# Kernel tuning notes

Hardware: AMD Instinct MI355X
Metric: run time of the kernel (lower is better)

## Reference

```python
import math
import jax, jax.numpy as jnp
import numpy as np

B, D, E, R, TOP_K = 16384, 2048, 64, 128, 2
TAU = 1.0
CAP_FACTOR = 1.25
TOP_C = min(E, max(4, 2 * TOP_K))  # GatingNetwork default top_c


def setup_inputs() -> dict:
    key = jax.random.key(0)
    ks = jax.random.split(key, 7)
    x = jax.random.normal(ks[0], (B, D), dtype=jnp.float32)
    # shared_encoder: nn.Linear(d, d) -> weight [out, in], bias [out]
    We = jax.random.normal(ks[1], (D, D), dtype=jnp.float32) / np.sqrt(D)
    be = jnp.zeros((D,), dtype=jnp.float32)
    # gating: nn.Linear(d, E, bias=False) -> weight [E, d]
    Wg = jax.random.normal(ks[2], (E, D), dtype=jnp.float32) / np.sqrt(D)
    # LowRankExpert per expert: U [r, d], V [d, r], gamma scalar (init 1.0)
    U = jax.random.normal(ks[3], (E, R, D), dtype=jnp.float32) / np.sqrt(D)
    V = jax.random.normal(ks[4], (E, D, R), dtype=jnp.float32) / np.sqrt(R)
    gamma = jnp.ones((E,), dtype=jnp.float32)
    return {"x": x, "We": We, "be": be, "Wg": Wg, "U": U, "V": V, "gamma": gamma}


def reference(x, We, be, Wg, U, V, gamma):
    # shared encoder
    enc = x @ We.T + be  # [B, D]

    # ---- gating: top-C candidates then top-K routing ----
    logits = (enc @ Wg.T) / TAU  # [B, E]
    topc_vals, topc_idx = jax.lax.top_k(logits, TOP_C)          # [B, C]
    topk_vals, pos_in_c = jax.lax.top_k(topc_vals, TOP_K)       # [B, K]
    topk_idx = jnp.take_along_axis(topc_idx, pos_in_c, axis=1)  # [B, K]
    # masked stable softmax over the K selected logits (with 1e-12 eps as in source)
    m = jnp.max(topk_vals, axis=-1, keepdims=True)
    ex = jnp.exp(topk_vals - m)
    w = ex / (jnp.sum(ex, axis=-1, keepdims=True) + 1e-12)      # [B, K]

    # ---- flatten assignments ----
    N = B * TOP_K
    tok = jnp.repeat(jnp.arange(B), TOP_K)   # [N]
    eid = topk_idx.reshape(-1)               # [N]
    wf = w.reshape(-1)                       # [N]
    wmask = wf > 1e-12

    # ---- capacity-based dispatch (sort/group equivalent, fixed shapes) ----
    cap = int(math.ceil(CAP_FACTOR * N / E))  # expert capacity
    onehot = ((eid[:, None] == jnp.arange(E)[None, :]) & wmask[:, None]).astype(jnp.int32)  # [N, E]
    pos = jnp.cumsum(onehot, axis=0) - onehot                      # position within expert
    pos_of = jnp.take_along_axis(pos, eid[:, None], axis=1)[:, 0]  # [N]
    valid = wmask & (pos_of < cap)
    slot = jnp.where(valid, pos_of, cap)  # overflow -> dummy slot (never occurs at this cap)

    # gather tokens to per-expert buffers [E, cap+1, D]
    xbuf = jnp.zeros((E, cap + 1, D), dtype=enc.dtype).at[eid, slot].set(enc[tok])

    # batched low-rank experts: delta = gamma * V @ silu(U @ x)
    h = jax.nn.silu(jnp.einsum('ecd,erd->ecr', xbuf, U))
    delta = jnp.einsum('ecr,edr->ecd', h, V) * gamma[:, None, None]  # [E, cap+1, D]

    # scatter-combine: y = enc + sum_k w_k * delta_k (residual handled since sum w = 1)
    dflat = delta[eid, slot]  # [N, D]
    y = enc.at[tok].add(jnp.where(valid, wf, 0.0)[:, None] * dflat)
    return y
```

## Files before the change

### kernel.cpp

```cpp
#include <hip/hip_runtime.h>
#include <math.h>

#define NTOK 16384
#define DDIM 2048
#define NEXP 64
#define RRANK 128
#define CAP 640

typedef __attribute__((ext_vector_type(8))) short bf16x8;
typedef __attribute__((ext_vector_type(4))) float f32x4;
typedef __attribute__((address_space(1))) const unsigned int gu32_t;
typedef __attribute__((address_space(3))) unsigned int lu32_t;

__device__ __forceinline__ void gload16(const void* g, void* l) {
  __builtin_amdgcn_global_load_lds((gu32_t*)g, (lu32_t*)l, 16, 0, 0);
}

__device__ __forceinline__ float silu_f(float v) {
  return v / (1.f + expf(-v));
}

__device__ __forceinline__ unsigned short f2bf(float f) {
  unsigned int u = __float_as_uint(f);
  unsigned int r = (u + 0x7fffu + ((u >> 16) & 1u)) >> 16;
  return (unsigned short)r;
}

__device__ __forceinline__ float bf2f(unsigned short u) {
  return __uint_as_float(((unsigned int)u) << 16);
}

__device__ __forceinline__ int swz256(int d) {
  return d ^ (((d >> 8) & 7) << 4);
}

__global__ __launch_bounds__(256) void cvt_all_kernel(
    const float* __restrict__ x, const float* __restrict__ We,
    const float* __restrict__ U, const float* __restrict__ V,
    unsigned short* __restrict__ xb, unsigned short* __restrict__ Web,
    unsigned short* __restrict__ Ub, unsigned short* __restrict__ Vb)
{
  const int S0 = NTOK * DDIM / 4;
  const int S1 = DDIM * DDIM / 4;
  const int S2 = NEXP * RRANK * DDIM / 4;
  const int total = S0 + S1 + 2 * S2;
  int i = blockIdx.x * 256 + threadIdx.x;
  const int stride = gridDim.x * 256;
  for (; i < total; i += stride) {
    const float* in; unsigned short* out; int j;
    if (i < S0) { in = x; out = xb; j = i; }
    else if (i < S0 + S1) { in = We; out = Web; j = i - S0; }
    else if (i < S0 + S1 + S2) { in = U; out = Ub; j = i - S0 - S1; }
    else { in = V; out = Vb; j = i - S0 - S1 - S2; }
    const float4 v = ((const float4*)in)[j];
    ushort4 o;
    o.x = f2bf(v.x); o.y = f2bf(v.y); o.z = f2bf(v.z); o.w = f2bf(v.w);
    ((ushort4*)out)[j] = o;
  }
}

__global__ __launch_bounds__(256) void enc_mfma4(
    const unsigned short* __restrict__ xb, const unsigned short* __restrict__ Web,
    const float* __restrict__ be, unsigned short* __restrict__ encbf)
{
  __shared__ unsigned short At[128 * 64];
  __shared__ unsigned short Bt[128 * 64];
  const int tid = threadIdx.x;
  const int lane = tid & 63, wid = tid >> 6;
  const int wr = wid >> 1, wc = wid & 1;
  const int fr = lane & 15, fq = lane >> 4;
  const int bid = blockIdx.x;
  const int wg = (bid & 7) * 256 + (bid >> 3);
  const int n0 = (wg & 15) * 128, m0 = (wg >> 4) * 128;

  const unsigned short* asrc[4];
  const unsigned short* bsrc[4];
  char* adst[4];
  char* bdst[4];
#pragma unroll
  for (int is = 0; is < 4; ++is) {
    const int doff = is * 4096 + tid * 16;
    const int r = doff >> 7;
    const int cs = ((doff >> 4) & 7) ^ (r & 7);
    asrc[is] = xb + (size_t)(m0 + r) * DDIM + cs * 8;
    bsrc[is] = Web + (size_t)(n0 + r) * DDIM + cs * 8;
    adst[is] = (char*)At + doff;
    bdst[is] = (char*)Bt + doff;
  }

  f32x4 acc[4][4];
#pragma unroll
  for (int m = 0; m < 4; ++m)
#pragma unroll
    for (int n = 0; n < 4; ++n) acc[m][n] = (f32x4){0.f, 0.f, 0.f, 0.f};

  for (int kb = 0; kb < DDIM; kb += 64) {
    __syncthreads();
#pragma unroll
    for (int is = 0; is < 4; ++is) {
      gload16(asrc[is] + kb, adst[is]);
      gload16(bsrc[is] + kb, bdst[is]);
    }
    __syncthreads();
#pragma unroll
    for (int kk = 0; kk < 2; ++kk) {
      bf16x8 af[4], bfv[4];
#pragma unroll
      for (int m = 0; m < 4; ++m) {
        const int row = wr * 64 + m * 16 + fr;
        af[m] = *(const bf16x8*)((const char*)At +
                 row * 128 + (((kk * 4 + fq) ^ (row & 7)) << 4));
      }
#pragma unroll
      for (int n = 0; n < 4; ++n) {
        const int row = wc * 64 + n * 16 + fr;
        bfv[n] = *(const bf16x8*)((const char*)Bt +
                  row * 128 + (((kk * 4 + fq) ^ (row & 7)) << 4));
      }
#pragma unroll
      for (int m = 0; m < 4; ++m)
#pragma unroll
        for (int n = 0; n < 4; ++n)
          acc[m][n] = __builtin_amdgcn_mfma_f32_16x16x32_bf16(af[m], bfv[n], acc[m][n], 0, 0, 0);
    }
  }

  float bias[4];
#pragma unroll
  for (int n = 0; n < 4; ++n) bias[n] = be[n0 + wc * 64 + n * 16 + fr];
#pragma unroll
  for (int m = 0; m < 4; ++m) {
#pragma unroll
    for (int j = 0; j < 4; ++j) {
      const int row = m0 + wr * 64 + m * 16 + fq * 4 + j;
      unsigned short* ob = encbf + (size_t)row * DDIM + n0 + wc * 64 + fr;
#pragma unroll
      for (int n = 0; n < 4; ++n)
        ob[n * 16] = f2bf(acc[m][n][j] + bias[n]);
    }
  }
}

__global__ __launch_bounds__(256) void gmat_part_kernel(
    const float* __restrict__ We, const float* __restrict__ Wg,
    double* __restrict__ Gpart)
{
  __shared__ float As[64][68];
  __shared__ float Bs[64][68];
  const int tid = threadIdx.x;
  const int d0 = blockIdx.x * 64;
  const int oc = blockIdx.y;
  const int tx = tid & 15, ty = tid >> 4;
  const int row = tid >> 2, p = (tid & 3) * 16;

  double acc[4][4];
#pragma unroll
  for (int j = 0; j < 4; ++j)
#pragma unroll
    for (int i = 0; i < 4; ++i) acc[j][i] = 0.0;

  for (int o0 = oc * 256; o0 < oc * 256 + 256; o0 += 64) {
    float4 wv[4], gv[4];
#pragma unroll
    for (int q = 0; q < 4; ++q) {
      wv[q] = *(const float4*)(We + (size_t)(o0 + row) * DDIM + d0 + p + q * 4);
      gv[q] = *(const float4*)(Wg + (size_t)row * DDIM + o0 + p + q * 4);
    }
    __syncthreads();
#pragma unroll
    for (int q = 0; q < 4; ++q) {
      const int c = p + q * 4;
      As[row][c + 0] = wv[q].x; As[row][c + 1] = wv[q].y;
      As[row][c + 2] = wv[q].z; As[row][c + 3] = wv[q].w;
      Bs[c + 0][row] = gv[q].x; Bs[c + 1][row] = gv[q].y;
      Bs[c + 2][row] = gv[q].z; Bs[c + 3][row] = gv[q].w;
    }
    __syncthreads();
#pragma unroll 8
    for (int oo = 0; oo < 64; ++oo) {
      double a[4], b[4];
#pragma unroll
      for (int j = 0; j < 4; ++j) a[j] = (double)As[oo][ty * 4 + j];
#pragma unroll
      for (int i = 0; i < 4; ++i) b[i] = (double)Bs[oo][tx * 4 + i];
#pragma unroll
      for (int j = 0; j < 4; ++j)
#pragma unroll
        for (int i = 0; i < 4; ++i)
          acc[j][i] = fma(a[j], b[i], acc[j][i]);
    }
    __syncthreads();
  }
#pragma unroll
  for (int j = 0; j < 4; ++j)
#pragma unroll
    for (int i = 0; i < 4; ++i) {
      const int d = d0 + ty * 4 + j, e = tx * 4 + i;
      Gpart[(size_t)oc * (DDIM * NEXP) + (size_t)e * DDIM + d] = acc[j][i];
    }
}

__global__ __launch_bounds__(256) void greduce_kernel(
    const double* __restrict__ Gpart, double* __restrict__ Gt,
    unsigned short* __restrict__ Gbf)
{
  const int idx = blockIdx.x * 256 + threadIdx.x;
  double s = 0.0;
#pragma unroll
  for (int oc = 0; oc < 8; ++oc)
    s += Gpart[(size_t)oc * (DDIM * NEXP) + idx];
  Gt[idx] = s;
  Gbf[idx] = f2bf((float)s);
}

__global__ __launch_bounds__(256) void bias_c_kernel(
    const float* __restrict__ be, const float* __restrict__ Wg,
    double* __restrict__ c64)
{
  const int e = blockIdx.x;
  const int tid = threadIdx.x;
  double s = 0.0;
  for (int o = tid; o < DDIM; o += 256)
    s += (double)be[o] * (double)Wg[(size_t)e * DDIM + o];
  __shared__ double red[256];
  red[tid] = s;
  __syncthreads();
  for (int st = 128; st > 0; st >>= 1) {
    if (tid < st) red[tid] += red[tid + st];
    __syncthreads();
  }
  if (tid == 0) c64[e] = red[0];
}

__global__ __launch_bounds__(256) void logits_topc_kernel(
    const unsigned short* __restrict__ xb, const unsigned short* __restrict__ Gbf,
    const double* __restrict__ c64, int* __restrict__ cand8)
{
  __shared__ unsigned short At[128 * 32];
  __shared__ unsigned short Bt[64 * 32];
  __shared__ float Ls[128][64];
  const int tid = threadIdx.x;
  const int lane = tid & 63, wid = tid >> 6;
  const int fr = lane & 15, fq = lane >> 4;
  const int t0 = blockIdx.x * 128;

  const int doff0 = wid * 1024 + lane * 16;
  const int doff1 = doff0 + 4096;
  const unsigned short* as0 = xb + (size_t)(t0 + (doff0 >> 6)) * DDIM + ((doff0 & 63) >> 1);
  const unsigned short* as1 = xb + (size_t)(t0 + (doff1 >> 6)) * DDIM + ((doff1 & 63) >> 1);
  const unsigned short* bs0 = Gbf + (size_t)(doff0 >> 6) * DDIM + ((doff0 & 63) >> 1);
  char* ad0 = (char*)At + doff0; char* ad1 = (char*)At + doff1;
  char* bd0 = (char*)Bt + doff0;

  f32x4 acc[2][4];
#pragma unroll
  for (int m = 0; m < 2; ++m)
#pragma unroll
    for (int n = 0; n < 4; ++n) acc[m][n] = (f32x4){0.f, 0.f, 0.f, 0.f};

  for (int kb = 0; kb < DDIM; kb += 32) {
    __syncthreads();
    gload16(as0 + kb, ad0);
    gload16(as1 + kb, ad1);
    gload16(bs0 + kb, bd0);
    __syncthreads();
    bf16x8 af[2], bfr[4];
#pragma unroll
    for (int m = 0; m < 2; ++m)
      af[m] = *(const bf16x8*)&At[(wid * 32 + m * 16 + fr) * 32 + fq * 8];
#pragma unroll
    for (int n = 0; n < 4; ++n)
      bfr[n] = *(const bf16x8*)&Bt[(n * 16 + fr) * 32 + fq * 8];
#pragma unroll
    for (int m = 0; m < 2; ++m)
#pragma unroll
      for (int n = 0; n < 4; ++n)
        acc[m][n] = __builtin_amdgcn_mfma_f32_16x16x32_bf16(af[m], bfr[n], acc[m][n], 0, 0, 0);
  }

#pragma unroll
  for (int m = 0; m < 2; ++m)
#pragma unroll
    for (int j = 0; j < 4; ++j) {
      const int row = wid * 32 + m * 16 + fq * 4 + j;
#pragma unroll
      for (int n = 0; n < 4; ++n)
        Ls[row][n * 16 + fr] = acc[m][n][j];
    }
  __syncthreads();

  if (tid < 128) {
    float v8[8];
    int i8[8];
#pragma unroll
    for (int c = 0; c < 8; ++c) { v8[c] = -INFINITY; i8[c] = 0; }
    for (int e = 0; e < NEXP; ++e) {
      const float v = Ls[tid][e] + (float)c64[e];
      if (v > v8[7]) {
        int p = 7;
        while (p > 0 && v > v8[p - 1]) { v8[p] = v8[p - 1]; i8[p] = i8[p - 1]; --p; }
        v8[p] = v; i8[p] = e;
      }
    }
    int* cp = cand8 + (size_t)(t0 + tid) * 8;
#pragma unroll
    for (int c = 0; c < 8; ++c) cp[c] = i8[c];
  }
}

__global__ __launch_bounds__(256) void refine_kernel(
    const float* __restrict__ x, const double* __restrict__ Gt,
    const double* __restrict__ c64, const int* __restrict__ cand8,
    int* __restrict__ topk, float* __restrict__ wkf)
{
  const int t = blockIdx.x;
  const int tid = threadIdx.x;
  const int lane = tid & 63, w = tid >> 6;
  __shared__ float xs[DDIM];
  __shared__ double red[8][4];

  ((float4*)xs)[tid] = ((const float4*)(x + (size_t)t * DDIM))[tid];
  ((float4*)xs)[tid + 256] = ((const float4*)(x + (size_t)t * DDIM))[tid + 256];
  __syncthreads();

  int myc[8];
#pragma unroll
  for (int c = 0; c < 8; ++c) myc[c] = cand8[(size_t)t * 8 + c];

#pragma unroll
  for (int c = 0; c < 8; ++c) {
    const double* g = Gt + (size_t)myc[c] * DDIM;
    double s = 0.0;
#pragma unroll
    for (int q = 0; q < 8; ++q) {
      const int d = q * 256 + tid;
      s += (double)xs[d] * g[d];
    }
#pragma unroll
    for (int off = 32; off > 0; off >>= 1) s += __shfl_down(s, off);
    if (lane == 0) red[c][w] = s;
  }
  __syncthreads();

  if (tid == 0) {
    double v1 = -1e300, v2 = -1e300;
    int i1 = 0, i2 = 0;
#pragma unroll
    for (int c = 0; c < 8; ++c) {
      const double v = red[c][0] + red[c][1] + red[c][2] + red[c][3] + c64[myc[c]];
      if (v > v1) { v2 = v1; i2 = i1; v1 = v; i1 = myc[c]; }
      else if (v > v2) { v2 = v; i2 = myc[c]; }
    }
    const double e2 = exp(v2 - v1);
    const double s = 1.0 + e2 + 1e-12;
    topk[2 * t] = i1; topk[2 * t + 1] = i2;
    wkf[2 * t] = (float)(1.0 / s);
    wkf[2 * t + 1] = (float)(e2 / s);
  }
}

__global__ __launch_bounds__(256) void route_kernel(
    const int* __restrict__ topk, const float* __restrict__ wkf,
    int* __restrict__ slots , int* __restrict__ counts_eff,
    int* __restrict__ val )
{
  const int e = blockIdx.x;
  const int tid = threadIdx.x;
  const int lane = tid & 63, wave = tid >> 6;
  __shared__ int wcnt[4];
  __shared__ int sbase;
  if (tid == 0) sbase = 0;
  __syncthreads();

  for (int c0 = 0; c0 < NTOK * 2; c0 += 256) {
    const int a = c0 + tid;
    const bool match = (topk[a] == e) && (wkf[a] > 1e-12f);
    const unsigned long long bal = __ballot(match);
    if (lane == 0) wcnt[wave] = __popcll(bal);
    __syncthreads();
    int base = sbase;
    for (int w = 0; w < 4; ++w)
      if (w < wave) base += wcnt[w];
    const int rank = base + (int)__popcll(bal & ((1ull << lane) - 1ull));
    if (match && rank < CAP) {
      slots[e * CAP + rank] = a;
      val[a] = 1;
    }
    __syncthreads();
    if (tid == 0) sbase += wcnt[0] + wcnt[1] + wcnt[2] + wcnt[3];
  }
  __syncthreads();
  if (tid == 0) counts_eff[e] = (sbase < CAP) ? sbase : CAP;
}

__global__ __launch_bounds__(256) void expert_fused(
    const unsigned short* __restrict__ encbf, const unsigned short* __restrict__ Ub,
    const unsigned short* __restrict__ Vb, const float* __restrict__ gamma,
    const int* __restrict__ counts_eff, const int* __restrict__ slots,
    const float* __restrict__ wkf, unsigned short* __restrict__ Dbuf)
{
  const int lin = blockIdx.x;
  const int wg = (lin & 7) * 80 + (lin >> 3);
  const int e = wg / 10;
  const int t0 = (wg % 10) * 64;
  const int cnt = counts_eff[e];
  if (t0 >= cnt) return;

  __shared__ int aid[64];
  __shared__ int toks[64];
  __shared__ float wts[64];
  __shared__ unsigned short Ht[64 * 128];
  __shared__ char U2[32768];

  const int tid = threadIdx.x;
  const int lane = tid & 63, wid = tid >> 6;
  const int wr = wid >> 1, wc = wid & 1;
  const int fr = lane & 15, fq = lane >> 4;

  if (tid < 64) {
    const int i = t0 + tid;
    if (i < cnt) {
      const int a = slots[e * CAP + i];
      aid[tid] = a;
      toks[tid] = a >> 1;
      wts[tid] = wkf[a] * gamma[e];
    } else {
      aid[tid] = -1;
      toks[tid] = slots[e * CAP] >> 1;
      wts[tid] = 0.f;
    }
  }
  __syncthreads();

  unsigned short* At = (unsigned short*)U2;
  unsigned short* Bt = (unsigned short*)(U2 + 8192);
  const unsigned short* Ue = Ub + (size_t)e * RRANK * DDIM;

  size_t aoff[2]; char* adst[2];
#pragma unroll
  for (int is = 0; is < 2; ++is) {
    const int doff = is * 4096 + tid * 16;
    const int r = doff >> 7;
    const int cs = ((doff >> 4) & 7) ^ (r & 7);
    aoff[is] = (size_t)toks[r] * DDIM + cs * 8;
    adst[is] = (char*)At + doff;
  }
  const unsigned short* bsrc[4]; char* bdst[4];
#pragma unroll
  for (int is = 0; is < 4; ++is) {
    const int doff = is * 4096 + tid * 16;
    const int r = doff >> 7;
    const int cs = ((doff >> 4) & 7) ^ (r & 7);
    bsrc[is] = Ue + (size_t)r * DDIM + cs * 8;
    bdst[is] = (char*)Bt + doff;
  }

  f32x4 hacc[2][4];
#pragma unroll
  for (int m = 0; m < 2; ++m)
#pragma unroll
    for (int n = 0; n < 4; ++n) hacc[m][n] = (f32x4){0.f, 0.f, 0.f, 0.f};

  for (int kb = 0; kb < DDIM; kb += 64) {
    __syncthreads();
    gload16(encbf + aoff[0] + kb, adst[0]);
    gload16(encbf + aoff[1] + kb, adst[1]);
#pragma unroll
    for (int is = 0; is < 4; ++is)
      gload16(bsrc[is] + kb, bdst[is]);
    __syncthreads();
#pragma unroll
    for (int kk = 0; kk < 2; ++kk) {
      bf16x8 af[2], bfv[4];
#pragma unroll
      for (int m = 0; m < 2; ++m) {
        const int row = wr * 32 + m * 16 + fr;
        af[m] = *(const bf16x8*)((const char*)At +
                 row * 128 + (((kk * 4 + fq) ^ (row & 7)) << 4));
      }
#pragma unroll
      for (int n = 0; n < 4; ++n) {
        const int row = wc * 64 + n * 16 + fr;
        bfv[n] = *(const bf16x8*)((const char*)Bt +
                  row * 128 + (((kk * 4 + fq) ^ (row & 7)) << 4));
      }
#pragma unroll
      for (int m = 0; m < 2; ++m)
#pragma unroll
        for (int n = 0; n < 4; ++n)
          hacc[m][n] = __builtin_amdgcn_mfma_f32_16x16x32_bf16(af[m], bfv[n], hacc[m][n], 0, 0, 0);
    }
  }

  __syncthreads();
#pragma unroll
  for (int m = 0; m < 2; ++m) {
#pragma unroll
    for (int j = 0; j < 4; ++j) {
      const int row = wr * 32 + m * 16 + fq * 4 + j;
#pragma unroll
      for (int n = 0; n < 4; ++n) {
        const int col = wc * 64 + n * 16 + fr;
        const int b = (row * 256 + col * 2) ^ ((row & 7) << 4);
        *(unsigned short*)((char*)Ht + b) = f2bf(silu_f(hacc[m][n][j]));
      }
    }
  }
  __syncthreads();

  unsigned short* Vt = (unsigned short*)U2;
  const unsigned short* Ve = Vb + (size_t)e * DDIM * RRANK;
  const int hd = tid * 16;

  bf16x8 paf[2][4];
  float wv[2][4];
  int av[2][4];
#pragma unroll
  for (int m = 0; m < 2; ++m) {
    const int row = wr * 32 + m * 16 + fr;
#pragma unroll
    for (int kk = 0; kk < 4; ++kk) {
      const int b = (row * 256 + kk * 64 + fq * 16) ^ ((row & 7) << 4);
      paf[m][kk] = *(const bf16x8*)((const char*)Ht + b);
    }
#pragma unroll
    for (int j = 0; j < 4; ++j) {
      const int tl = wr * 32 + m * 16 + fq * 4 + j;
      wv[m][j] = wts[tl];
      av[m][j] = aid[tl];
    }
  }

  for (int nb = 0; nb < 16; ++nb) {
    __syncthreads();
    const unsigned short* vsrc = Ve + (size_t)nb * 128 * RRANK;
#pragma unroll
    for (int is = 0; is < 8; ++is) {
      const int d = is * 4096 + hd;
      gload16(vsrc + (swz256(d) >> 1), (char*)Vt + d);
    }
    __syncthreads();

    f32x4 acc[2][4];
#pragma unroll
    for (int m = 0; m < 2; ++m)
#pragma unroll
      for (int n = 0; n < 4; ++n) acc[m][n] = (f32x4){0.f, 0.f, 0.f, 0.f};

#pragma unroll
    for (int n = 0; n < 4; ++n) {
      const int drow = wc * 64 + n * 16 + fr;
#pragma unroll
      for (int kk = 0; kk < 4; ++kk) {
        const int b = (drow * 256 + kk * 64 + fq * 16) ^ ((drow & 7) << 4);
        const bf16x8 bfr = *(const bf16x8*)((const char*)Vt + b);
#pragma unroll
        for (int m = 0; m < 2; ++m)
          acc[m][n] = __builtin_amdgcn_mfma_f32_16x16x32_bf16(paf[m][kk], bfr, acc[m][n], 0, 0, 0);
      }
    }

#pragma unroll
    for (int m = 0; m < 2; ++m) {
#pragma unroll
      for (int j = 0; j < 4; ++j) {
        if (av[m][j] >= 0) {
          const float w = wv[m][j];
          unsigned short* dp = Dbuf + (size_t)av[m][j] * DDIM + nb * 128 + wc * 64 + fr;
#pragma unroll
          for (int n = 0; n < 4; ++n)
            dp[n * 16] = f2bf(acc[m][n][j] * w);
        }
      }
    }
  }
}

__global__ __launch_bounds__(256) void combine_kernel(
    const unsigned short* __restrict__ encbf, const unsigned short* __restrict__ Dbuf,
    const int* __restrict__ val, float* __restrict__ y)
{
  const int t = blockIdx.x;
  const int tid = threadIdx.x;
  const int c0 = tid * 8;
  float* yp = y + (size_t)t * DDIM + c0;
  const int v0 = val[2 * t], v1 = val[2 * t + 1];

  const ushort4 e0 = *(const ushort4*)(encbf + (size_t)t * DDIM + c0);
  const ushort4 e1 = *(const ushort4*)(encbf + (size_t)t * DDIM + c0 + 4);
  float o[8] = {bf2f(e0.x), bf2f(e0.y), bf2f(e0.z), bf2f(e0.w),
                bf2f(e1.x), bf2f(e1.y), bf2f(e1.z), bf2f(e1.w)};

  if (v0) {
    const ushort4 d0 = *(const ushort4*)(Dbuf + (size_t)(2 * t) * DDIM + c0);
    const ushort4 d1 = *(const ushort4*)(Dbuf + (size_t)(2 * t) * DDIM + c0 + 4);
    o[0] += bf2f(d0.x); o[1] += bf2f(d0.y); o[2] += bf2f(d0.z); o[3] += bf2f(d0.w);
    o[4] += bf2f(d1.x); o[5] += bf2f(d1.y); o[6] += bf2f(d1.z); o[7] += bf2f(d1.w);
  }
  if (v1) {
    const ushort4 d0 = *(const ushort4*)(Dbuf + (size_t)(2 * t + 1) * DDIM + c0);
    const ushort4 d1 = *(const ushort4*)(Dbuf + (size_t)(2 * t + 1) * DDIM + c0 + 4);
    o[0] += bf2f(d0.x); o[1] += bf2f(d0.y); o[2] += bf2f(d0.z); o[3] += bf2f(d0.w);
    o[4] += bf2f(d1.x); o[5] += bf2f(d1.y); o[6] += bf2f(d1.z); o[7] += bf2f(d1.w);
  }
  *(float4*)(yp) = (float4){o[0], o[1], o[2], o[3]};
  *(float4*)(yp + 4) = (float4){o[4], o[5], o[6], o[7]};
}

extern "C" void kernel_launch(void* const* d_in, const int* in_sizes, int n_in,
                              void* d_out, int out_size, void* d_ws, size_t ws_size,
                              hipStream_t stream)
{
  const float* x     = (const float*)d_in[0];
  const float* We    = (const float*)d_in[1];
  const float* be    = (const float*)d_in[2];
  const float* Wg    = (const float*)d_in[3];
  const float* U     = (const float*)d_in[4];
  const float* V     = (const float*)d_in[5];
  const float* gamma = (const float*)d_in[6];
  float* y = (float*)d_out;

  char* ws = (char*)d_ws;
  int*            topk       = (int*)(ws + 0);
  float*          wkf        = (float*)(ws + 131072);
  int*            counts_eff = (int*)(ws + 262144);
  double*         c64        = (double*)(ws + 262400);
  int*            cand8      = (int*)(ws + 262912);
  double*         Gt         = (double*)(ws + 787200);
  unsigned short* G_bf       = (unsigned short*)(ws + 1835776);
  int*            slots      = (int*)(ws + 2097920);
  int*            val        = (int*)(ws + 2261760);
  unsigned short* Dbuf       = (unsigned short*)(ws + 2392832);
  unsigned short* x_bf       = (unsigned short*)(ws + 2392832);
  unsigned short* We_bf      = (unsigned short*)(ws + 69501696);
  double*         Gpart      = (double*)(ws + 77890304);
  unsigned short* U_bf       = (unsigned short*)(ws + 136610560);
  unsigned short* V_bf       = (unsigned short*)(ws + 170164992);
  unsigned short* enc_bf     = (unsigned short*)(ws + 203719424);

  hipMemsetAsync(val, 0, 131072, stream);

  cvt_all_kernel<<<dim3(2048), 256, 0, stream>>>(x, We, U, V, x_bf, We_bf, U_bf, V_bf);

  gmat_part_kernel<<<dim3(32, 8), 256, 0, stream>>>(We, Wg, Gpart);
  greduce_kernel<<<dim3(512), 256, 0, stream>>>(Gpart, Gt, G_bf);
  bias_c_kernel<<<dim3(64), 256, 0, stream>>>(be, Wg, c64);
  logits_topc_kernel<<<dim3(128), 256, 0, stream>>>(x_bf, G_bf, c64, cand8);
  refine_kernel<<<dim3(NTOK), 256, 0, stream>>>(x, Gt, c64, cand8, topk, wkf);
  route_kernel<<<dim3(64), 256, 0, stream>>>(topk, wkf, slots, counts_eff, val);

  enc_mfma4<<<dim3(2048), 256, 0, stream>>>(x_bf, We_bf, be, enc_bf);
  expert_fused<<<dim3(640), 256, 0, stream>>>(enc_bf, U_bf, V_bf, gamma, counts_eff, slots, wkf, Dbuf);
  combine_kernel<<<dim3(NTOK), 256, 0, stream>>>(enc_bf, Dbuf, val, y);
}
```

Measured before the change: 742.3 us.

## Load V fragments straight to registers and make routing two-pass without barriers

The expert kernel's second GEMM now reads V fragments directly from global memory into registers for each 128-column block. This replaces the LDS staging through async global_load_lds and the two barriers per iteration, and the shared buffer shrinks so occupancy can rise. The route kernel now counts matches per wave in a first pass, then assigns ranks in a second pass with no per-chunk syncthreads, at the cost of reading topk and wkf twice. The direct loads skip the LDS swizzle and may be less coalesced; each wave fetches V separately, so global traffic rises.

```diff
diff --git a/kernel.cpp b/kernel.cpp
--- a/kernel.cpp
+++ b/kernel.cpp
@@ -28,10 +28,6 @@
 
 __device__ __forceinline__ float bf2f(unsigned short u) {
   return __uint_as_float(((unsigned int)u) << 16);
-}
-
-__device__ __forceinline__ int swz256(int d) {
-  return d ^ (((d >> 8) & 7) << 4);
 }
 
 __global__ __launch_bounds__(256) void cvt_all_kernel(
@@ -367,30 +363,35 @@
   const int e = blockIdx.x;
   const int tid = threadIdx.x;
   const int lane = tid & 63, wave = tid >> 6;
+  const int base0 = wave * 8192;
   __shared__ int wcnt[4];
-  __shared__ int sbase;
-  if (tid == 0) sbase = 0;
-  __syncthreads();
-
-  for (int c0 = 0; c0 < NTOK * 2; c0 += 256) {
-    const int a = c0 + tid;
+
+  int cnt = 0;
+  for (int c = 0; c < 8192; c += 64) {
+    const int a = base0 + c + lane;
+    const bool match = (topk[a] == e) && (wkf[a] > 1e-12f);
+    cnt += (int)__popcll(__ballot(match));
+  }
+  if (lane == 0) wcnt[wave] = cnt;
+  __syncthreads();
+
+  int run = 0;
+  for (int w = 0; w < 4; ++w)
+    if (w < wave) run += wcnt[w];
+  const int total = wcnt[0] + wcnt[1] + wcnt[2] + wcnt[3];
+
+  for (int c = 0; c < 8192; c += 64) {
+    const int a = base0 + c + lane;
     const bool match = (topk[a] == e) && (wkf[a] > 1e-12f);
     const unsigned long long bal = __ballot(match);
-    if (lane == 0) wcnt[wave] = __popcll(bal);
-    __syncthreads();
-    int base = sbase;
-    for (int w = 0; w < 4; ++w)
-      if (w < wave) base += wcnt[w];
-    const int rank = base + (int)__popcll(bal & ((1ull << lane) - 1ull));
+    const int rank = run + (int)__popcll(bal & ((1ull << lane) - 1ull));
     if (match && rank < CAP) {
       slots[e * CAP + rank] = a;
       val[a] = 1;
     }
-    __syncthreads();
-    if (tid == 0) sbase += wcnt[0] + wcnt[1] + wcnt[2] + wcnt[3];
-  }
-  __syncthreads();
-  if (tid == 0) counts_eff[e] = (sbase < CAP) ? sbase : CAP;
+    run += (int)__popcll(bal);
+  }
+  if (tid == 0) counts_eff[e] = (total < CAP) ? total : CAP;
 }
 
 __global__ __launch_bounds__(256) void expert_fused(
@@ -410,7 +411,7 @@
   __shared__ int toks[64];
   __shared__ float wts[64];
   __shared__ unsigned short Ht[64 * 128];
-  __shared__ char U2[32768];
+  __shared__ char U2[24576];
 
   const int tid = threadIdx.x;
   const int lane = tid & 63, wid = tid >> 6;
@@ -508,9 +509,7 @@
   }
   __syncthreads();
 
-  unsigned short* Vt = (unsigned short*)U2;
   const unsigned short* Ve = Vb + (size_t)e * DDIM * RRANK;
-  const int hd = tid * 16;
 
   bf16x8 paf[2][4];
   float wv[2][4];
@@ -531,15 +530,17 @@
     }
   }
 
+#pragma unroll 1
   for (int nb = 0; nb < 16; ++nb) {
-    __syncthreads();
-    const unsigned short* vsrc = Ve + (size_t)nb * 128 * RRANK;
-#pragma unroll
-    for (int is = 0; is < 8; ++is) {
-      const int d = is * 4096 + hd;
-      gload16(vsrc + (swz256(d) >> 1), (char*)Vt + d);
-    }
-    __syncthreads();
+    bf16x8 bfr[4][4];
+#pragma unroll
+    for (int n = 0; n < 4; ++n) {
+      const int drow = nb * 128 + wc * 64 + n * 16 + fr;
+      const unsigned short* vp = Ve + (size_t)drow * RRANK + fq * 8;
+#pragma unroll
+      for (int kk = 0; kk < 4; ++kk)
+        bfr[n][kk] = *(const bf16x8*)(vp + kk * 32);
+    }
 
     f32x4 acc[2][4];
 #pragma unroll
@@ -548,17 +549,12 @@
       for (int n = 0; n < 4; ++n) acc[m][n] = (f32x4){0.f, 0.f, 0.f, 0.f};
 
 #pragma unroll
-    for (int n = 0; n < 4; ++n) {
-      const int drow = wc * 64 + n * 16 + fr;
-#pragma unroll
-      for (int kk = 0; kk < 4; ++kk) {
-        const int b = (drow * 256 + kk * 64 + fq * 16) ^ ((drow & 7) << 4);
-        const bf16x8 bfr = *(const bf16x8*)((const char*)Vt + b);
+    for (int n = 0; n < 4; ++n)
+#pragma unroll
+      for (int kk = 0; kk < 4; ++kk)
 #pragma unroll
         for (int m = 0; m < 2; ++m)
-          acc[m][n] = __builtin_amdgcn_mfma_f32_16x16x32_bf16(paf[m][kk], bfr, acc[m][n], 0, 0, 0);
-      }
-    }
+          acc[m][n] = __builtin_amdgcn_mfma_f32_16x16x32_bf16(paf[m][kk], bfr[n][kk], acc[m][n], 0, 0, 0);
 
 #pragma unroll
     for (int m = 0; m < 2; ++m) {
```

New measurement: 785.5 us. +5.8%, slower.
